# Kernel optimization log

Measured on AMD Instinct MI355X. Metric: run time of the kernel, lower is better.

Reference implementation:

```python
import jax, jax.numpy as jnp
import numpy as np

N_PATCH, N_Z, K, BS = 16, 128, 10, 1024
D = N_PATCH * N_Z


def setup_inputs() -> dict:
    key = jax.random.key(0)
    k1, k2, k3, k4 = jax.random.split(key, 4)
    z = jax.random.normal(k1, (BS, D), dtype=jnp.float32)
    m = jax.random.normal(k2, (K, D), dtype=jnp.float32)
    L = jax.random.normal(k3, (K, D, D), dtype=jnp.float32)
    components = jax.random.randint(k4, (BS,), 0, K, dtype=jnp.int64)
    return {"z": z, "m": m, "L": L, "components": components}


def reference(z, m, L, components):
    # samps[k] = m[k] + z @ L[k].T   -> (K, BS, D)
    samps = jnp.einsum('bd,ked->kbe', z, L) + m[:, None, :]
    # one-hot mask-and-sum over components == gather selected expert per sample
    x = samps[components, jnp.arange(z.shape[0])]  # (BS, D)
    return x.reshape(-1, N_PATCH, N_Z)
```

## Files before the change

### kernel.cpp

```cpp
#include <hip/hip_runtime.h>
#include <hip/hip_bf16.h>


#define DDIM  2048
#define BSAMP 1024
#define KCOMP 10
#define MPAD  160
#define NT    64
#define BK    32
#define ZBYTES (MPAD * BK * 4)
#define LBYTES (NT * BK * 4)
#define STAGE_BYTES (ZBYTES + LBYTES)

typedef __attribute__((ext_vector_type(8))) short bf16x8;
typedef __attribute__((ext_vector_type(4))) float f32x4;

__device__ __forceinline__ void async16(void* lds, const void* g) {
    __builtin_amdgcn_global_load_lds(
        (const __attribute__((address_space(1))) void*)g,
        (__attribute__((address_space(3))) void*)lds, 16, 0, 0);
}

__device__ __forceinline__ short bfs(float x) {
    __hip_bfloat16 h = __float2bfloat16(x);
    return *reinterpret_cast<short*>(&h);
}

__device__ __forceinline__ bf16x8 frag8(const char* base, int o0, int o1) {
    f32x4 x = *(const f32x4*)(base + o0);
    f32x4 y = *(const f32x4*)(base + o1);
    bf16x8 r;
#pragma unroll
    for (int i = 0; i < 4; ++i) { r[i] = bfs(x[i]); r[4 + i] = bfs(y[i]); }
    return r;
}

__global__ void build_map(const int* __restrict__ comp,
                          int* __restrict__ rowmap,
                          int* __restrict__ counts) {
    __shared__ int sc[KCOMP];
    const int t = threadIdx.x;
    if (t < KCOMP) sc[t] = 0;
    __syncthreads();
    const int c = comp[t];
    const int r = atomicAdd(&sc[c], 1);
    if (r < MPAD) rowmap[c * MPAD + r] = t;
    __syncthreads();
    if (t < KCOMP) counts[t] = sc[t];
}

__global__ __launch_bounds__(256, 2)
void gmm_gemm(const float* __restrict__ z,
              const float* __restrict__ mvec,
              const float* __restrict__ Lmat,
              const int* __restrict__ rowmap,
              const int* __restrict__ counts,
              float* __restrict__ out) {
    __shared__ __attribute__((aligned(16))) char smem[2 * STAGE_BYTES];
    const int t    = threadIdx.x;
    const int lane = t & 63;
    const int w    = t >> 6;
    const int mh   = w >> 1;
    const int nh   = w & 1;
    const int k    = blockIdx.y;
    const int n0   = blockIdx.x * NT;
    const float* Lk = Lmat + (size_t)k * DDIM * DDIM;

    const int rq   = t >> 3;
    const int scol = ((t & 7) ^ (rq & 7)) * 4;
    int rm[5];
#pragma unroll
    for (int j = 0; j < 5; ++j)
        rm[j] = rowmap[k * MPAD + j * 32 + rq] & (BSAMP - 1);
    const unsigned ub = (unsigned)(t & ~63) * 16;

    auto stage = [&](int buf, int it) {
        char* lb = smem + buf * STAGE_BYTES;
        const int d0 = it * BK + scol;
#pragma unroll
        for (int j = 0; j < 5; ++j)
            async16(lb + j * 4096 + ub, z + (size_t)rm[j] * DDIM + d0);
        async16(lb + ZBYTES + ub,        Lk + (size_t)(n0 + rq) * DDIM + d0);
        async16(lb + ZBYTES + 4096 + ub, Lk + (size_t)(n0 + 32 + rq) * DDIM + d0);
    };

    f32x4 acc[5][2];
#pragma unroll
    for (int mt = 0; mt < 5; ++mt)
#pragma unroll
        for (int nt = 0; nt < 2; ++nt) acc[mt][nt] = (f32x4){0.f, 0.f, 0.f, 0.f};

    stage(0, 0);
    __syncthreads();

    const int fr = lane & 15;
    const int g0 = (lane >> 4) * 2;

    for (int it = 0; it < DDIM / BK; ++it) {
        if (it + 1 < DDIM / BK) stage((it + 1) & 1, it + 1);
        const char* lb = smem + (it & 1) * STAGE_BYTES;

        const int rb0 = nh * 32 + fr;
        const int rb1 = rb0 + 16;
        bf16x8 b0 = frag8(lb + ZBYTES,
                          rb0 * 128 + ((g0 ^ rb0) & 7) * 16,
                          rb0 * 128 + (((g0 + 1) ^ rb0) & 7) * 16);
        bf16x8 b1 = frag8(lb + ZBYTES,
                          rb1 * 128 + ((g0 ^ rb1) & 7) * 16,
                          rb1 * 128 + (((g0 + 1) ^ rb1) & 7) * 16);
#pragma unroll
        for (int mt = 0; mt < 5; ++mt) {
            const int ra = mh * 80 + mt * 16 + fr;
            bf16x8 a = frag8(lb,
                             ra * 128 + ((g0 ^ ra) & 7) * 16,
                             ra * 128 + (((g0 + 1) ^ ra) & 7) * 16);
            acc[mt][0] = __builtin_amdgcn_mfma_f32_16x16x32_bf16(a, b0, acc[mt][0], 0, 0, 0);
            acc[mt][1] = __builtin_amdgcn_mfma_f32_16x16x32_bf16(a, b1, acc[mt][1], 0, 0, 0);
        }
        __syncthreads();
    }

    const int cnt   = counts[k];
    const int rquad = (lane >> 4) * 4;
#pragma unroll
    for (int nt = 0; nt < 2; ++nt) {
        const int e = n0 + nh * 32 + nt * 16 + fr;
        const float mu = mvec[k * DDIM + e];
#pragma unroll
        for (int mt = 0; mt < 5; ++mt) {
            const int sb = mh * 80 + mt * 16 + rquad;
#pragma unroll
            for (int r = 0; r < 4; ++r) {
                const int slot = sb + r;
                if (slot < cnt) {
                    const int b = rowmap[k * MPAD + slot];
                    out[(size_t)b * DDIM + e] = acc[mt][nt][r] + mu;
                }
            }
        }
    }
}

extern "C" void kernel_launch(void* const* d_in, const int* in_sizes, int n_in,
                              void* d_out, int out_size, void* d_ws, size_t ws_size,
                              hipStream_t stream) {
    const float* z    = (const float*)d_in[0];
    const float* mvec = (const float*)d_in[1];
    const float* Lmat = (const float*)d_in[2];
    const int* comp   = (const int*)d_in[3];
    float* out        = (float*)d_out;

    int* rowmap = (int*)d_ws;
    int* counts = rowmap + KCOMP * MPAD;

    build_map<<<1, BSAMP, 0, stream>>>(comp, rowmap, counts);
    gmm_gemm<<<dim3(DDIM / NT, KCOMP), 256, 0, stream>>>(z, mvec, Lmat, rowmap,
                                                         counts, out);
}
```

Baseline: 272.2 us.

## Pre-convert z to bf16 once and stage bf16 z tiles in the GEMM

Adds a separate pass that converts z to bf16 into the workspace. The GEMM then stages bf16 z rows, which halves z LDS and global traffic, removes the per-iteration fp32-to-bf16 conversion of A fragments, and uses a new LDS swizzle. Z rows beyond the component's count are no longer staged, and launch bounds are raised to 4 blocks per CU for more occupancy. It costs an extra kernel launch and a pass over z, and falls back to the old kernel when the workspace is too small.

Result: no change. 274.8 us (+1.0%).

```diff
diff --git a/kernel.cpp b/kernel.cpp
--- a/kernel.cpp
+++ b/kernel.cpp
@@ -8,9 +8,8 @@
 #define MPAD  160
 #define NT    64
 #define BK    32
-#define ZBYTES (MPAD * BK * 4)
-#define LBYTES (NT * BK * 4)
-#define STAGE_BYTES (ZBYTES + LBYTES)
+#define ZREG  10240
+#define STAGE 18432
 
 typedef __attribute__((ext_vector_type(8))) short bf16x8;
 typedef __attribute__((ext_vector_type(4))) float f32x4;
@@ -20,15 +19,13 @@
         (const __attribute__((address_space(1))) void*)g,
         (__attribute__((address_space(3))) void*)lds, 16, 0, 0);
 }
-
 __device__ __forceinline__ short bfs(float x) {
     __hip_bfloat16 h = __float2bfloat16(x);
     return *reinterpret_cast<short*>(&h);
 }
-
-__device__ __forceinline__ bf16x8 frag8(const char* base, int o0, int o1) {
-    f32x4 x = *(const f32x4*)(base + o0);
-    f32x4 y = *(const f32x4*)(base + o1);
+__device__ __forceinline__ bf16x8 packB(const char* rowb, int o0, int o1) {
+    f32x4 x = *(const f32x4*)(rowb + o0);
+    f32x4 y = *(const f32x4*)(rowb + o1);
     bf16x8 r;
 #pragma unroll
     for (int i = 0; i < 4; ++i) { r[i] = bfs(x[i]); r[4 + i] = bfs(y[i]); }
@@ -49,79 +46,179 @@
     if (t < KCOMP) counts[t] = sc[t];
 }
 
+__global__ void zconv(const float* __restrict__ z, short* __restrict__ zb) {
+    const int i = (blockIdx.x * 256 + threadIdx.x) * 8;
+    f32x4 a = *(const f32x4*)(z + i);
+    f32x4 b = *(const f32x4*)(z + i + 4);
+    bf16x8 o;
+#pragma unroll
+    for (int j = 0; j < 4; ++j) { o[j] = bfs(a[j]); o[4 + j] = bfs(b[j]); }
+    *(bf16x8*)(zb + i) = o;
+}
+
+__device__ __forceinline__ int swz(int r) { return (r & 3) ^ ((r >> 2) & 3); }
+
+__global__ __launch_bounds__(256, 4)
+void gmm_bf16z(const short* __restrict__ zb,
+               const float* __restrict__ mvec,
+               const float* __restrict__ Lmat,
+               const int* __restrict__ rowmap,
+               const int* __restrict__ counts,
+               float* __restrict__ out) {
+    __shared__ __attribute__((aligned(16))) char smem[2 * STAGE];
+    const int t = threadIdx.x, lane = t & 63;
+    const int w = t >> 6, mh = w >> 1, nh = w & 1;
+    const int k = blockIdx.y, n0 = blockIdx.x * NT;
+    const float* Lk = Lmat + (size_t)k * DDIM * DDIM;
+    const int cnt = counts[k];
+
+    const int zq = t >> 2, zcs = t & 3;
+    const int zr1 = 64 + zq, zr2 = 128 + zq;
+    const int rmB = k * MPAD;
+    const int rm0 = rowmap[rmB + zq] & (BSAMP - 1);
+    const int rm1 = rowmap[rmB + zr1] & (BSAMP - 1);
+    const int rm2 = rowmap[rmB + ((zr2 < MPAD) ? zr2 : 0)] & (BSAMP - 1);
+    const short* zp0 = zb + (size_t)rm0 * DDIM + (zcs ^ swz(zq)) * 8;
+    const short* zp1 = zb + (size_t)rm1 * DDIM + (zcs ^ swz(zr1)) * 8;
+    const short* zp2 = zb + (size_t)rm2 * DDIM + (zcs ^ swz(zr2)) * 8;
+    const int lcs = t & 7;
+    const int lr2 = (t >= 128) ? ((t - 128) >> 3) : 0;
+    const int lr3 = 16 + (t >> 3);
+    const int lr4 = 48 + (t >> 3);
+    const float* lp2 = Lk + (size_t)(n0 + lr2) * DDIM + (lcs ^ (lr2 & 7)) * 4;
+    const float* lp3 = Lk + (size_t)(n0 + lr3) * DDIM + (lcs ^ (lr3 & 7)) * 4;
+    const float* lp4 = Lk + (size_t)(n0 + (lr4 & 63)) * DDIM + (lcs ^ (lr4 & 7)) * 4;
+    const int ub  = (t & ~63) << 4;
+    const int ubh = ((t - 128) & ~63) << 4;
+    const bool lowHalf = (t < 128);
+    const bool st1 = (cnt > 64), st2 = (cnt > 128);
+
+    auto stage = [&](int buf, int it) {
+        char* lb = smem + buf * STAGE;
+        const int d = it * BK;
+        async16(lb + ub, zp0 + d);
+        if (st1) async16(lb + 4096 + ub, zp1 + d);
+        if (lowHalf) {
+            if (st2) async16(lb + 8192 + ub, zp2 + d);
+            async16(lb + ZREG + 6144 + ub, lp4 + d);
+        } else {
+            async16(lb + ZREG + ubh, lp2 + d);
+        }
+        async16(lb + ZREG + 2048 + ub, lp3 + d);
+    };
+
+    f32x4 acc[5][2];
+#pragma unroll
+    for (int mt = 0; mt < 5; ++mt)
+#pragma unroll
+        for (int nt = 0; nt < 2; ++nt) acc[mt][nt] = (f32x4){0.f, 0.f, 0.f, 0.f};
+
+    stage(0, 0);
+    __syncthreads();
+
+    const int fr = lane & 15, g = lane >> 4;
+    const int szA   = (fr & 3) ^ ((fr >> 2) & 3);
+    const int aoff  = ((g ^ szA) & 3) * 16;
+    const int boff0 = (((g * 2)     ^ (fr & 7)) & 7) * 16;
+    const int boff1 = (((g * 2 + 1) ^ (fr & 7)) & 7) * 16;
+    const int rb0 = (nh * 32 + fr) * 128, rb1 = (nh * 32 + 16 + fr) * 128;
+    const int raB = (mh * 80 + fr) * 64;
+
+    for (int it = 0; it < DDIM / BK; ++it) {
+        if (it + 1 < DDIM / BK) stage((it + 1) & 1, it + 1);
+        const char* lb = smem + (it & 1) * STAGE;
+        const char* Lb = lb + ZREG;
+        bf16x8 b0 = packB(Lb + rb0, boff0, boff1);
+        bf16x8 b1 = packB(Lb + rb1, boff0, boff1);
+#pragma unroll
+        for (int mt = 0; mt < 5; ++mt) {
+            bf16x8 a = *(const bf16x8*)(lb + raB + mt * 16 * 64 + aoff);
+            acc[mt][0] = __builtin_amdgcn_mfma_f32_16x16x32_bf16(a, b0, acc[mt][0], 0, 0, 0);
+            acc[mt][1] = __builtin_amdgcn_mfma_f32_16x16x32_bf16(a, b1, acc[mt][1], 0, 0, 0);
+        }
+        __syncthreads();
+    }
+
+    const int rquad = (lane >> 4) * 4;
+#pragma unroll
+    for (int nt = 0; nt < 2; ++nt) {
+        const int e = n0 + nh * 32 + nt * 16 + fr;
+        const float mu = mvec[k * DDIM + e];
+#pragma unroll
+        for (int mt = 0; mt < 5; ++mt) {
+            const int sb = mh * 80 + mt * 16 + rquad;
+#pragma unroll
+            for (int r = 0; r < 4; ++r) {
+                const int slot = sb + r;
+                if (slot < cnt) {
+                    const int b = rowmap[rmB + slot];
+                    out[(size_t)b * DDIM + e] = acc[mt][nt][r] + mu;
+                }
+            }
+        }
+    }
+}
+
+__device__ __forceinline__ bf16x8 frag8(const char* base, int o0, int o1) {
+    f32x4 x = *(const f32x4*)(base + o0);
+    f32x4 y = *(const f32x4*)(base + o1);
+    bf16x8 r;
+#pragma unroll
+    for (int i = 0; i < 4; ++i) { r[i] = bfs(x[i]); r[4 + i] = bfs(y[i]); }
+    return r;
+}
 __global__ __launch_bounds__(256, 2)
-void gmm_gemm(const float* __restrict__ z,
-              const float* __restrict__ mvec,
-              const float* __restrict__ Lmat,
-              const int* __restrict__ rowmap,
-              const int* __restrict__ counts,
-              float* __restrict__ out) {
-    __shared__ __attribute__((aligned(16))) char smem[2 * STAGE_BYTES];
-    const int t    = threadIdx.x;
-    const int lane = t & 63;
-    const int w    = t >> 6;
-    const int mh   = w >> 1;
-    const int nh   = w & 1;
-    const int k    = blockIdx.y;
-    const int n0   = blockIdx.x * NT;
+void gmm_f32z(const float* __restrict__ z, const float* __restrict__ mvec,
+              const float* __restrict__ Lmat, const int* __restrict__ rowmap,
+              const int* __restrict__ counts, float* __restrict__ out) {
+    __shared__ __attribute__((aligned(16))) char smem[2 * 28672];
+    const int t = threadIdx.x, lane = t & 63, w = t >> 6;
+    const int mh = w >> 1, nh = w & 1;
+    const int k = blockIdx.y, n0 = blockIdx.x * NT;
     const float* Lk = Lmat + (size_t)k * DDIM * DDIM;
-
-    const int rq   = t >> 3;
+    const int rq = t >> 3;
     const int scol = ((t & 7) ^ (rq & 7)) * 4;
     int rm[5];
 #pragma unroll
     for (int j = 0; j < 5; ++j)
         rm[j] = rowmap[k * MPAD + j * 32 + rq] & (BSAMP - 1);
     const unsigned ub = (unsigned)(t & ~63) * 16;
-
     auto stage = [&](int buf, int it) {
-        char* lb = smem + buf * STAGE_BYTES;
-        const int d0 = it * BK + scol;
+        char* lb = smem + buf * 28672;
+        const int d0 = it * 32 + scol;
 #pragma unroll
         for (int j = 0; j < 5; ++j)
             async16(lb + j * 4096 + ub, z + (size_t)rm[j] * DDIM + d0);
-        async16(lb + ZBYTES + ub,        Lk + (size_t)(n0 + rq) * DDIM + d0);
-        async16(lb + ZBYTES + 4096 + ub, Lk + (size_t)(n0 + 32 + rq) * DDIM + d0);
+        async16(lb + 20480 + ub,        Lk + (size_t)(n0 + rq) * DDIM + d0);
+        async16(lb + 20480 + 4096 + ub, Lk + (size_t)(n0 + 32 + rq) * DDIM + d0);
     };
-
     f32x4 acc[5][2];
 #pragma unroll
     for (int mt = 0; mt < 5; ++mt)
 #pragma unroll
         for (int nt = 0; nt < 2; ++nt) acc[mt][nt] = (f32x4){0.f, 0.f, 0.f, 0.f};
-
     stage(0, 0);
     __syncthreads();
-
-    const int fr = lane & 15;
-    const int g0 = (lane >> 4) * 2;
-
-    for (int it = 0; it < DDIM / BK; ++it) {
-        if (it + 1 < DDIM / BK) stage((it + 1) & 1, it + 1);
-        const char* lb = smem + (it & 1) * STAGE_BYTES;
-
-        const int rb0 = nh * 32 + fr;
-        const int rb1 = rb0 + 16;
-        bf16x8 b0 = frag8(lb + ZBYTES,
-                          rb0 * 128 + ((g0 ^ rb0) & 7) * 16,
+    const int fr = lane & 15, g0 = (lane >> 4) * 2;
+    for (int it = 0; it < DDIM / 32; ++it) {
+        if (it + 1 < DDIM / 32) stage((it + 1) & 1, it + 1);
+        const char* lb = smem + (it & 1) * 28672;
+        const int rb0 = nh * 32 + fr, rb1 = rb0 + 16;
+        bf16x8 b0 = frag8(lb + 20480, rb0 * 128 + ((g0 ^ rb0) & 7) * 16,
                           rb0 * 128 + (((g0 + 1) ^ rb0) & 7) * 16);
-        bf16x8 b1 = frag8(lb + ZBYTES,
-                          rb1 * 128 + ((g0 ^ rb1) & 7) * 16,
+        bf16x8 b1 = frag8(lb + 20480, rb1 * 128 + ((g0 ^ rb1) & 7) * 16,
                           rb1 * 128 + (((g0 + 1) ^ rb1) & 7) * 16);
 #pragma unroll
         for (int mt = 0; mt < 5; ++mt) {
             const int ra = mh * 80 + mt * 16 + fr;
-            bf16x8 a = frag8(lb,
-                             ra * 128 + ((g0 ^ ra) & 7) * 16,
+            bf16x8 a = frag8(lb, ra * 128 + ((g0 ^ ra) & 7) * 16,
                              ra * 128 + (((g0 + 1) ^ ra) & 7) * 16);
             acc[mt][0] = __builtin_amdgcn_mfma_f32_16x16x32_bf16(a, b0, acc[mt][0], 0, 0, 0);
             acc[mt][1] = __builtin_amdgcn_mfma_f32_16x16x32_bf16(a, b1, acc[mt][1], 0, 0, 0);
         }
         __syncthreads();
     }
-
-    const int cnt   = counts[k];
-    const int rquad = (lane >> 4) * 4;
+    const int cnt = counts[k], rquad = (lane >> 4) * 4;
 #pragma unroll
     for (int nt = 0; nt < 2; ++nt) {
         const int e = n0 + nh * 32 + nt * 16 + fr;
@@ -132,10 +229,8 @@
 #pragma unroll
             for (int r = 0; r < 4; ++r) {
                 const int slot = sb + r;
-                if (slot < cnt) {
-                    const int b = rowmap[k * MPAD + slot];
-                    out[(size_t)b * DDIM + e] = acc[mt][nt][r] + mu;
-                }
+                if (slot < cnt)
+                    out[(size_t)rowmap[k * MPAD + slot] * DDIM + e] = acc[mt][nt][r] + mu;
             }
         }
     }
@@ -152,8 +247,16 @@
 
     int* rowmap = (int*)d_ws;
     int* counts = rowmap + KCOMP * MPAD;
-
     build_map<<<1, BSAMP, 0, stream>>>(comp, rowmap, counts);
-    gmm_gemm<<<dim3(DDIM / NT, KCOMP), 256, 0, stream>>>(z, mvec, Lmat, rowmap,
-                                                         counts, out);
-}
+
+    const size_t need = 8192 + (size_t)BSAMP * DDIM * 2;
+    if (ws_size >= need) {
+        short* zbuf = (short*)((char*)d_ws + 8192);
+        zconv<<<BSAMP * DDIM / (256 * 8), 256, 0, stream>>>(z, zbuf);
+        gmm_bf16z<<<dim3(DDIM / NT, KCOMP), 256, 0, stream>>>(
+            zbuf, mvec, Lmat, rowmap, counts, out);
+    } else {
+        gmm_f32z<<<dim3(DDIM / NT, KCOMP), 256, 0, stream>>>(
+            z, mvec, Lmat, rowmap, counts, out);
+    }
+}
```

## Pre-pack gathered z into bf16 MFMA fragments and stream L directly

Applied to the files above, without the earlier changes.

Adds a zprep kernel that gathers each component's rows of z, converts them to bf16, and writes them in MFMA fragment order into workspace. A new LDS-free kernel then reads A fragments straight from that buffer and L directly from global memory, converting L to bf16 in registers. The grid is split by component half, with an early exit and a template specialisation on the number of occupied 16-row tiles, so empty or partly empty row tiles are skipped. The old LDS-staged kernel is kept as a fallback when the workspace is too small. The cost is an extra kernel launch and a workspace round trip for z, and L reads are no longer coalesced through shared memory.

Result: slower. 287.0 us (+5.4%).

```diff
diff --git a/kernel.cpp b/kernel.cpp
--- a/kernel.cpp
+++ b/kernel.cpp
@@ -6,33 +6,13 @@
 #define BSAMP 1024
 #define KCOMP 10
 #define MPAD  160
-#define NT    64
-#define BK    32
-#define ZBYTES (MPAD * BK * 4)
-#define LBYTES (NT * BK * 4)
-#define STAGE_BYTES (ZBYTES + LBYTES)
 
 typedef __attribute__((ext_vector_type(8))) short bf16x8;
 typedef __attribute__((ext_vector_type(4))) float f32x4;
-
-__device__ __forceinline__ void async16(void* lds, const void* g) {
-    __builtin_amdgcn_global_load_lds(
-        (const __attribute__((address_space(1))) void*)g,
-        (__attribute__((address_space(3))) void*)lds, 16, 0, 0);
-}
 
 __device__ __forceinline__ short bfs(float x) {
     __hip_bfloat16 h = __float2bfloat16(x);
     return *reinterpret_cast<short*>(&h);
-}
-
-__device__ __forceinline__ bf16x8 frag8(const char* base, int o0, int o1) {
-    f32x4 x = *(const f32x4*)(base + o0);
-    f32x4 y = *(const f32x4*)(base + o1);
-    bf16x8 r;
-#pragma unroll
-    for (int i = 0; i < 4; ++i) { r[i] = bfs(x[i]); r[4 + i] = bfs(y[i]); }
-    return r;
 }
 
 __global__ void build_map(const int* __restrict__ comp,
@@ -49,79 +29,169 @@
     if (t < KCOMP) counts[t] = sc[t];
 }
 
+__global__ void zprep(const float* __restrict__ z,
+                      const int* __restrict__ rowmap,
+                      short* __restrict__ zfrag) {
+    const int idx  = blockIdx.x * 256 + threadIdx.x;
+    const int lane = idx & 63;
+    const int rest = idx >> 6;
+    const int ms   = rest % 10;
+    const int kit  = rest / 10;
+    const int it   = kit & 63;
+    const int k    = kit >> 6;
+    const int slot = ms * 16 + (lane & 15);
+    const int r    = rowmap[k * MPAD + slot] & (BSAMP - 1);
+    const int d    = it * 32 + (lane >> 4) * 8;
+    const float* zp = z + (size_t)r * DDIM + d;
+    f32x4 a = *(const f32x4*)zp;
+    f32x4 b = *(const f32x4*)(zp + 4);
+    bf16x8 o;
+#pragma unroll
+    for (int j = 0; j < 4; ++j) { o[j] = bfs(a[j]); o[4 + j] = bfs(b[j]); }
+    *(bf16x8*)(zfrag + (size_t)idx * 8) = o;
+}
+
+template <int MT>
+__device__ __forceinline__ void gmm_body(
+        const short* __restrict__ Ab,
+        const float* __restrict__ Bp,
+        const float* __restrict__ mvec,
+        const int* __restrict__ rowmap,
+        float* __restrict__ out,
+        int k, int mh, int e, int cnt, int lane) {
+    f32x4 acc[MT];
+#pragma unroll
+    for (int mt = 0; mt < MT; ++mt) acc[mt] = (f32x4){0.f, 0.f, 0.f, 0.f};
+
+#pragma unroll 2
+    for (int it = 0; it < DDIM / 32; ++it) {
+        f32x4 bx = *(const f32x4*)(Bp);
+        f32x4 by = *(const f32x4*)(Bp + 4);
+        bf16x8 b;
+#pragma unroll
+        for (int j = 0; j < 4; ++j) { b[j] = bfs(bx[j]); b[4 + j] = bfs(by[j]); }
+#pragma unroll
+        for (int mt = 0; mt < MT; ++mt) {
+            bf16x8 a = *(const bf16x8*)(Ab + mt * 512);
+            acc[mt] = __builtin_amdgcn_mfma_f32_16x16x32_bf16(a, b, acc[mt], 0, 0, 0);
+        }
+        Ab += 5120;
+        Bp += 32;
+    }
+
+    const float mu  = mvec[k * DDIM + e];
+    const int rquad = (lane >> 4) * 4;
+    const int rmB   = k * MPAD;
+#pragma unroll
+    for (int mt = 0; mt < MT; ++mt) {
+        const int sb = mh * 80 + mt * 16 + rquad;
+#pragma unroll
+        for (int r = 0; r < 4; ++r) {
+            const int slot = sb + r;
+            if (slot < cnt) {
+                const int bidx = rowmap[rmB + slot];
+                out[(size_t)bidx * DDIM + e] = acc[mt][r] + mu;
+            }
+        }
+    }
+}
+
+__global__ __launch_bounds__(128, 4)
+void gmm_direct(const short* __restrict__ zfrag,
+                const float* __restrict__ mvec,
+                const float* __restrict__ Lmat,
+                const int* __restrict__ rowmap,
+                const int* __restrict__ counts,
+                float* __restrict__ out) {
+    const int t = threadIdx.x, lane = t & 63, nh = t >> 6;
+    const int n  = blockIdx.x;
+    const int k  = blockIdx.y;
+    const int mh = blockIdx.z;
+    const int cnt = counts[k];
+    const int rem = cnt - mh * 80;
+    if (rem <= 0) return;
+    const int nmt = (rem >= 80) ? 5 : ((rem + 15) >> 4);
+
+    const int e = n * 32 + nh * 16 + (lane & 15);
+    const short* Ab = zfrag + ((size_t)(k * 64) * 10 + mh * 5) * 512 + lane * 8;
+    const float* Bp = Lmat + (size_t)k * DDIM * DDIM + (size_t)e * DDIM
+                    + (lane >> 4) * 8;
+
+    switch (nmt) {
+        case 5: gmm_body<5>(Ab, Bp, mvec, rowmap, out, k, mh, e, cnt, lane); break;
+        case 4: gmm_body<4>(Ab, Bp, mvec, rowmap, out, k, mh, e, cnt, lane); break;
+        case 3: gmm_body<3>(Ab, Bp, mvec, rowmap, out, k, mh, e, cnt, lane); break;
+        case 2: gmm_body<2>(Ab, Bp, mvec, rowmap, out, k, mh, e, cnt, lane); break;
+        default: gmm_body<1>(Ab, Bp, mvec, rowmap, out, k, mh, e, cnt, lane); break;
+    }
+}
+
+typedef bf16x8 bf8_t;
+__device__ __forceinline__ void async16(void* lds, const void* g) {
+    __builtin_amdgcn_global_load_lds(
+        (const __attribute__((address_space(1))) void*)g,
+        (__attribute__((address_space(3))) void*)lds, 16, 0, 0);
+}
+__device__ __forceinline__ bf16x8 frag8(const char* base, int o0, int o1) {
+    f32x4 x = *(const f32x4*)(base + o0);
+    f32x4 y = *(const f32x4*)(base + o1);
+    bf16x8 r;
+#pragma unroll
+    for (int i = 0; i < 4; ++i) { r[i] = bfs(x[i]); r[4 + i] = bfs(y[i]); }
+    return r;
+}
 __global__ __launch_bounds__(256, 2)
-void gmm_gemm(const float* __restrict__ z,
-              const float* __restrict__ mvec,
-              const float* __restrict__ Lmat,
-              const int* __restrict__ rowmap,
-              const int* __restrict__ counts,
-              float* __restrict__ out) {
-    __shared__ __attribute__((aligned(16))) char smem[2 * STAGE_BYTES];
-    const int t    = threadIdx.x;
-    const int lane = t & 63;
-    const int w    = t >> 6;
-    const int mh   = w >> 1;
-    const int nh   = w & 1;
-    const int k    = blockIdx.y;
-    const int n0   = blockIdx.x * NT;
+void gmm_f32z(const float* __restrict__ z, const float* __restrict__ mvec,
+              const float* __restrict__ Lmat, const int* __restrict__ rowmap,
+              const int* __restrict__ counts, float* __restrict__ out) {
+    __shared__ __attribute__((aligned(16))) char smem[2 * 28672];
+    const int t = threadIdx.x, lane = t & 63, w = t >> 6;
+    const int mh = w >> 1, nh = w & 1;
+    const int k = blockIdx.y, n0 = blockIdx.x * 64;
     const float* Lk = Lmat + (size_t)k * DDIM * DDIM;
-
-    const int rq   = t >> 3;
+    const int rq = t >> 3;
     const int scol = ((t & 7) ^ (rq & 7)) * 4;
     int rm[5];
 #pragma unroll
     for (int j = 0; j < 5; ++j)
         rm[j] = rowmap[k * MPAD + j * 32 + rq] & (BSAMP - 1);
     const unsigned ub = (unsigned)(t & ~63) * 16;
-
     auto stage = [&](int buf, int it) {
-        char* lb = smem + buf * STAGE_BYTES;
-        const int d0 = it * BK + scol;
+        char* lb = smem + buf * 28672;
+        const int d0 = it * 32 + scol;
 #pragma unroll
         for (int j = 0; j < 5; ++j)
             async16(lb + j * 4096 + ub, z + (size_t)rm[j] * DDIM + d0);
-        async16(lb + ZBYTES + ub,        Lk + (size_t)(n0 + rq) * DDIM + d0);
-        async16(lb + ZBYTES + 4096 + ub, Lk + (size_t)(n0 + 32 + rq) * DDIM + d0);
+        async16(lb + 20480 + ub,        Lk + (size_t)(n0 + rq) * DDIM + d0);
+        async16(lb + 20480 + 4096 + ub, Lk + (size_t)(n0 + 32 + rq) * DDIM + d0);
     };
-
     f32x4 acc[5][2];
 #pragma unroll
     for (int mt = 0; mt < 5; ++mt)
 #pragma unroll
         for (int nt = 0; nt < 2; ++nt) acc[mt][nt] = (f32x4){0.f, 0.f, 0.f, 0.f};
-
     stage(0, 0);
     __syncthreads();
-
-    const int fr = lane & 15;
-    const int g0 = (lane >> 4) * 2;
-
-    for (int it = 0; it < DDIM / BK; ++it) {
-        if (it + 1 < DDIM / BK) stage((it + 1) & 1, it + 1);
-        const char* lb = smem + (it & 1) * STAGE_BYTES;
-
-        const int rb0 = nh * 32 + fr;
-        const int rb1 = rb0 + 16;
-        bf16x8 b0 = frag8(lb + ZBYTES,
-                          rb0 * 128 + ((g0 ^ rb0) & 7) * 16,
+    const int fr = lane & 15, g0 = (lane >> 4) * 2;
+    for (int it = 0; it < DDIM / 32; ++it) {
+        if (it + 1 < DDIM / 32) stage((it + 1) & 1, it + 1);
+        const char* lb = smem + (it & 1) * 28672;
+        const int rb0 = nh * 32 + fr, rb1 = rb0 + 16;
+        bf16x8 b0 = frag8(lb + 20480, rb0 * 128 + ((g0 ^ rb0) & 7) * 16,
                           rb0 * 128 + (((g0 + 1) ^ rb0) & 7) * 16);
-        bf16x8 b1 = frag8(lb + ZBYTES,
-                          rb1 * 128 + ((g0 ^ rb1) & 7) * 16,
+        bf16x8 b1 = frag8(lb + 20480, rb1 * 128 + ((g0 ^ rb1) & 7) * 16,
                           rb1 * 128 + (((g0 + 1) ^ rb1) & 7) * 16);
 #pragma unroll
         for (int mt = 0; mt < 5; ++mt) {
             const int ra = mh * 80 + mt * 16 + fr;
-            bf16x8 a = frag8(lb,
-                             ra * 128 + ((g0 ^ ra) & 7) * 16,
+            bf16x8 a = frag8(lb, ra * 128 + ((g0 ^ ra) & 7) * 16,
                              ra * 128 + (((g0 + 1) ^ ra) & 7) * 16);
             acc[mt][0] = __builtin_amdgcn_mfma_f32_16x16x32_bf16(a, b0, acc[mt][0], 0, 0, 0);
             acc[mt][1] = __builtin_amdgcn_mfma_f32_16x16x32_bf16(a, b1, acc[mt][1], 0, 0, 0);
         }
         __syncthreads();
     }
-
-    const int cnt   = counts[k];
-    const int rquad = (lane >> 4) * 4;
+    const int cnt = counts[k], rquad = (lane >> 4) * 4;
 #pragma unroll
     for (int nt = 0; nt < 2; ++nt) {
         const int e = n0 + nh * 32 + nt * 16 + fr;
@@ -132,10 +202,8 @@
 #pragma unroll
             for (int r = 0; r < 4; ++r) {
                 const int slot = sb + r;
-                if (slot < cnt) {
-                    const int b = rowmap[k * MPAD + slot];
-                    out[(size_t)b * DDIM + e] = acc[mt][nt][r] + mu;
-                }
+                if (slot < cnt)
+                    out[(size_t)rowmap[k * MPAD + slot] * DDIM + e] = acc[mt][nt][r] + mu;
             }
         }
     }
@@ -152,8 +220,18 @@
 
     int* rowmap = (int*)d_ws;
     int* counts = rowmap + KCOMP * MPAD;
-
     build_map<<<1, BSAMP, 0, stream>>>(comp, rowmap, counts);
-    gmm_gemm<<<dim3(DDIM / NT, KCOMP), 256, 0, stream>>>(z, mvec, Lmat, rowmap,
-                                                         counts, out);
-}
+
+    const size_t zf_off = 8192;
+    const size_t zf_sz  = (size_t)KCOMP * 64 * 10 * 64 * 16;
+
+    if (ws_size >= zf_off + zf_sz) {
+        short* zfrag = (short*)((char*)d_ws + zf_off);
+        zprep<<<1600, 256, 0, stream>>>(z, rowmap, zfrag);
+        gmm_direct<<<dim3(64, KCOMP, 2), 128, 0, stream>>>(
+            zfrag, mvec, Lmat, rowmap, counts, out);
+    } else {
+        gmm_f32z<<<dim3(32, KCOMP), 256, 0, stream>>>(
+            z, mvec, Lmat, rowmap, counts, out);
+    }
+}
```
